# Kernel tuning notes

Measured on AMD Instinct MI355X. Metric: run time of the kernel, lower is better.

## Reference

```python
import jax, jax.numpy as jnp
import numpy as np
import math

B, L, D = 2, 2048, 1024
H, HD = 16, 64          # num heads, head dim
R = 256                 # kv lora rank = D // 4
E, K, F = 8, 2, 1024    # routed experts, top_k, intermediate size


def rmsnorm(x, w, eps=1e-6):
    ms = jnp.mean(x * x, axis=-1, keepdims=True)
    return w * (x * jax.lax.rsqrt(ms + eps))


def setup_inputs() -> dict:
    key = jax.random.key(0)
    ks = jax.random.split(key, 16)
    s = 0.02
    return {
        "x": jax.random.normal(ks[0], (B, L, D), jnp.float32),
        "ln1_w": jnp.ones((D,), jnp.float32),
        "q_w": jax.random.normal(ks[1], (D, H * HD), jnp.float32) * s,
        "kvd_w": jax.random.normal(ks[2], (D, R), jnp.float32) * s,
        "kvn_w": jnp.ones((R,), jnp.float32),
        "kvu_w": jax.random.normal(ks[3], (R, 2 * H * HD), jnp.float32) * s,
        "o_w": jax.random.normal(ks[4], (H * HD, D), jnp.float32) * s,
        "ln2_w": jnp.ones((D,), jnp.float32),
        "gate_w": jax.random.normal(ks[5], (D, E), jnp.float32) * s,
        "sh_w1": jax.random.normal(ks[6], (D, F), jnp.float32) * s,
        "sh_w2": jax.random.normal(ks[7], (F, D), jnp.float32) * s,
        "sh_w3": jax.random.normal(ks[8], (D, F), jnp.float32) * s,
        "re_w1": jax.random.normal(ks[9], (E, D, F), jnp.float32) * s,
        "re_w2": jax.random.normal(ks[10], (E, F, D), jnp.float32) * s,
        "re_w3": jax.random.normal(ks[11], (E, D, F), jnp.float32) * s,
    }


def reference(x, ln1_w, q_w, kvd_w, kvn_w, kvu_w, o_w, ln2_w, gate_w,
              sh_w1, sh_w2, sh_w3, re_w1, re_w2, re_w3):
    # ---- MLHA attention with pre-RMSNorm and latent-compressed KV ----
    xn = rmsnorm(x, ln1_w)
    q = (xn @ q_w).reshape(B, L, H, HD)
    latent = rmsnorm(xn @ kvd_w, kvn_w)                 # [B,L,R]
    kv = latent @ kvu_w                                 # [B,L,2*H*HD]
    k, v = jnp.split(kv, 2, axis=-1)
    k = k.reshape(B, L, H, HD)
    v = v.reshape(B, L, H, HD)
    scores = jnp.einsum('bxhd,byhd->bhxy', q, k) / math.sqrt(HD)
    causal = jnp.tril(jnp.ones((L, L), bool))
    scores = jnp.where(causal, scores, -jnp.inf)
    attn = jax.nn.softmax(scores, axis=-1)
    attn_out = jnp.einsum('bhxy,byhd->bxhd', attn, v).reshape(B, L, H * HD)
    h = x + attn_out @ o_w

    # ---- MoE (inference: no jitter, expert_bias = 0, no bias update) ----
    hn = rmsnorm(h, ln2_w)
    flat = hn.reshape(-1, D)                            # [T,D], T=B*L
    # shared expert (SwiGLU)
    shared = (jax.nn.silu(flat @ sh_w1) * (flat @ sh_w3)) @ sh_w2
    # router
    logits = flat @ gate_w                              # [T,E]
    probs = jax.nn.softmax(logits, axis=-1)
    topw, topi = jax.lax.top_k(probs, K)                # [T,K]
    topw = topw / jnp.sum(topw, axis=-1, keepdims=True)
    # per-token per-expert combine weight [T,E]
    combine = jnp.sum(topw[..., None] * jax.nn.one_hot(topi, E, dtype=flat.dtype), axis=1)
    # all routed experts densely, then masked combine (same math as masked loop)
    h1 = jnp.einsum('td,edf->etf', flat, re_w1)
    h3 = jnp.einsum('td,edf->etf', flat, re_w3)
    eo = jnp.einsum('etf,efd->etd', jax.nn.silu(h1) * h3, re_w2)
    routed = jnp.einsum('te,etd->td', combine, eo)
    moe_out = (shared + routed).reshape(B, L, D)
    return h + moe_out, probs
```

## Files before the change

kernel.cpp:

```cpp
#include <hip/hip_runtime.h>
#include <hip/hip_bf16.h>
#include <cstdint>
#include <cstddef>

typedef unsigned short u16;
typedef unsigned int u32;
typedef __attribute__((ext_vector_type(8))) short bf16x8;
typedef __attribute__((ext_vector_type(4))) float f32x4;

static constexpr int Bb = 2, Ll = 2048, Dd = 1024, Hh = 16, Rr = 256, Ee = 8, Ff = 1024;
static constexpr int Tt = Bb * Ll;
static constexpr float QSCALE = 0.18033688011112042f;

__device__ __forceinline__ u16 f2bf(float f){
  union { float f; u32 u; } v; v.f = f;
  u32 u = v.u;
  u32 r = u + 0x7FFFu + ((u >> 16) & 1u);
  return (u16)(r >> 16);
}
__device__ __forceinline__ float bf2f(u16 b){
  union { u32 u; float f; } v; v.u = ((u32)b) << 16; return v.f;
}

#define GLDS(gp, lp) __builtin_amdgcn_global_load_lds( \
    (const __attribute__((address_space(1))) unsigned int*)(gp), \
    (__attribute__((address_space(3))) unsigned int*)(lp), 16, 0, 0)

__global__ void transpose5(const float* __restrict__ q_w, const float* __restrict__ o_w,
                           const float* __restrict__ w1, const float* __restrict__ w3,
                           const float* __restrict__ w2,
                           u16* __restrict__ qkvdT, u16* __restrict__ oT,
                           u16* __restrict__ sh13T, u16* __restrict__ sh2T){
  const float* s; u16* d; int off, str;
  switch (blockIdx.z){
    case 0: s = q_w; d = qkvdT; off = 0; str = 1; break;
    case 1: s = o_w; d = oT;    off = 0; str = 1; break;
    case 2: s = w1;  d = sh13T; off = 0; str = 2; break;
    case 3: s = w3;  d = sh13T; off = 1; str = 2; break;
    default: s = w2; d = sh2T;  off = 0; str = 1; break;
  }
  __shared__ float tile[32][33];
  int bx = blockIdx.x * 32, by = blockIdx.y * 32;
  int tx = threadIdx.x, ty = threadIdx.y;
  #pragma unroll
  for (int i = ty; i < 32; i += 8) tile[i][tx] = s[(size_t)(by + i) * 1024 + bx + tx];
  __syncthreads();
  #pragma unroll
  for (int i = ty; i < 32; i += 8)
    d[(size_t)(off + (bx + i) * str) * 1024 + by + tx] = f2bf(tile[tx][i]);
}

__global__ void transposeEx(const float* __restrict__ re_w1, const float* __restrict__ re_w3,
                            const float* __restrict__ re_w2,
                            u16* __restrict__ re13T, u16* __restrict__ re2T){
  int z = blockIdx.z, which = z >> 3, e = z & 7;
  const float* s; u16* d; int off, str;
  size_t eo = (size_t)e * 1024 * 1024;
  if (which == 0){ s = re_w1 + eo; d = re13T + (size_t)e * 2048 * 1024; off = 0; str = 2; }
  else if (which == 1){ s = re_w3 + eo; d = re13T + (size_t)e * 2048 * 1024; off = 1; str = 2; }
  else { s = re_w2 + eo; d = re2T + (size_t)e * 1024 * 1024; off = 0; str = 1; }
  __shared__ float tile[32][33];
  int bx = blockIdx.x * 32, by = blockIdx.y * 32;
  int tx = threadIdx.x, ty = threadIdx.y;
  #pragma unroll
  for (int i = ty; i < 32; i += 8) tile[i][tx] = s[(size_t)(by + i) * 1024 + bx + tx];
  __syncthreads();
  #pragma unroll
  for (int i = ty; i < 32; i += 8)
    d[(size_t)(off + (bx + i) * str) * 1024 + by + tx] = f2bf(tile[tx][i]);
}

__global__ void transpose_conv(const float* __restrict__ src, u16* __restrict__ dst,
                               int K, int N, int dstOff){
  __shared__ float tile[32][33];
  int bx = blockIdx.x * 32, by = blockIdx.y * 32;
  int tx = threadIdx.x, ty = threadIdx.y;
  #pragma unroll
  for (int i = ty; i < 32; i += 8) tile[i][tx] = src[(size_t)(by + i) * N + bx + tx];
  __syncthreads();
  #pragma unroll
  for (int i = ty; i < 32; i += 8)
    dst[(size_t)(dstOff + bx + i) * K + by + tx] = f2bf(tile[tx][i]);
}

template<int DIM>
__global__ void rmsnorm_kernel(const float* __restrict__ x, const float* __restrict__ w,
                               u16* __restrict__ out){
  int t = blockIdx.x;
  const float* xr = x + (size_t)t * DIM;
  u16* orow = out + (size_t)t * DIM;
  int tid = threadIdx.x;
  constexpr int NT = 256;
  constexpr int PER = DIM / NT > 0 ? DIM / NT : 1;
  float vals[PER];
  float ss = 0.f;
  #pragma unroll
  for (int i = 0; i < PER; i++){
    int d = tid + i * NT;
    float v = (d < DIM) ? xr[d] : 0.f;
    vals[i] = v; ss += v * v;
  }
  __shared__ float red[4];
  for (int m = 32; m; m >>= 1) ss += __shfl_xor(ss, m, 64);
  if ((tid & 63) == 0) red[tid >> 6] = ss;
  __syncthreads();
  float tot = red[0] + red[1] + red[2] + red[3];
  float rn = rsqrtf(tot / DIM + 1e-6f);
  #pragma unroll
  for (int i = 0; i < PER; i++){
    int d = tid + i * NT;
    if (d < DIM) orow[d] = f2bf(vals[i] * rn * w[d]);
  }
}

__global__ void router_kernel(const float* __restrict__ h, const float* __restrict__ ln2w,
                              const float* __restrict__ gate,
                              float* __restrict__ probs_out,
                              int* __restrict__ topi, float* __restrict__ topw,
                              u16* __restrict__ hn){
  int t = blockIdx.x; int tid = threadIdx.x;
  const float* hr = h + (size_t)t * Dd;
  float v[4]; float ss = 0.f;
  #pragma unroll
  for (int i = 0; i < 4; i++){ float x = hr[tid + i * 256]; v[i] = x; ss += x * x; }
  __shared__ float red[4];
  for (int m = 32; m; m >>= 1) ss += __shfl_xor(ss, m, 64);
  if ((tid & 63) == 0) red[tid >> 6] = ss;
  __syncthreads();
  float rn = rsqrtf((red[0] + red[1] + red[2] + red[3]) / Dd + 1e-6f);
  float p[8];
  #pragma unroll
  for (int e = 0; e < 8; e++) p[e] = 0.f;
  #pragma unroll
  for (int i = 0; i < 4; i++){
    int d = tid + i * 256;
    float hv = v[i] * rn * ln2w[d];
    hn[(size_t)t * Dd + d] = f2bf(hv);
    const float* g = gate + (size_t)d * 8;
    #pragma unroll
    for (int e = 0; e < 8; e++) p[e] += hv * g[e];
  }
  #pragma unroll
  for (int e = 0; e < 8; e++){
    float x = p[e];
    for (int m = 32; m; m >>= 1) x += __shfl_xor(x, m, 64);
    p[e] = x;
  }
  __shared__ float pe[4][8];
  if ((tid & 63) == 0){ for (int e = 0; e < 8; e++) pe[tid >> 6][e] = p[e]; }
  __syncthreads();
  if (tid == 0){
    float lg[8];
    for (int e = 0; e < 8; e++) lg[e] = pe[0][e] + pe[1][e] + pe[2][e] + pe[3][e];
    float mx = lg[0];
    for (int e = 1; e < 8; e++) mx = fmaxf(mx, lg[e]);
    float pr[8]; float s = 0.f;
    for (int e = 0; e < 8; e++){ pr[e] = __expf(lg[e] - mx); s += pr[e]; }
    float inv = 1.f / s;
    for (int e = 0; e < 8; e++) probs_out[(size_t)t * 8 + e] = pr[e] * inv;
    int i0 = 0;
    for (int e = 1; e < 8; e++) if (pr[e] > pr[i0]) i0 = e;
    int i1 = -1;
    for (int e = 0; e < 8; e++){ if (e == i0) continue; if (i1 < 0 || pr[e] > pr[i1]) i1 = e; }
    float w0 = pr[i0], w1 = pr[i1]; float wn = 1.f / (w0 + w1);
    topi[t * 2] = i0; topi[t * 2 + 1] = i1;
    topw[t * 2] = w0 * wn; topw[t * 2 + 1] = w1 * wn;
  }
}

__global__ void hist_kernel(const int* __restrict__ topi, int* __restrict__ counts){
  __shared__ int h[8];
  int tid = threadIdx.x;
  if (tid < 8) h[tid] = 0;
  __syncthreads();
  int base = blockIdx.x * 512;
  for (int i = tid; i < 512; i += 256) atomicAdd(&h[topi[base + i]], 1);
  __syncthreads();
  if (tid < 8) atomicAdd(&counts[tid], h[tid]);
}

__global__ void bucket_kernel(const int* __restrict__ topi, const float* __restrict__ topw,
                              const int* __restrict__ counts, int* __restrict__ cur,
                              int* __restrict__ entries, float* __restrict__ ew){
  __shared__ int lh[8], lbase[8], lcur[8], loffs[8];
  int tid = threadIdx.x;
  if (tid < 8) lh[tid] = 0;
  __syncthreads();
  int t = blockIdx.x * 256 + tid;
  int e0 = topi[t * 2], e1 = topi[t * 2 + 1];
  atomicAdd(&lh[e0], 1); atomicAdd(&lh[e1], 1);
  __syncthreads();
  if (tid == 0){
    int c = 0;
    for (int e = 0; e < 8; e++){ loffs[e] = c; c += counts[e]; }
  }
  if (tid < 8){ lbase[tid] = atomicAdd(&cur[tid], lh[tid]); lcur[tid] = 0; }
  __syncthreads();
  int p0 = atomicAdd(&lcur[e0], 1);
  int pos0 = loffs[e0] + lbase[e0] + p0;
  entries[pos0] = t; ew[pos0] = topw[t * 2];
  int p1 = atomicAdd(&lcur[e1], 1);
  int pos1 = loffs[e1] + lbase[e1] + p1;
  entries[pos1] = t; ew[pos1] = topw[t * 2 + 1];
}

template<int TM, int ROWMODE, int MODE>
__launch_bounds__(256)
__global__ void gemm_bt(const u16* __restrict__ A, const u16* __restrict__ Bt,
                        void* __restrict__ C, const float* __restrict__ res,
                        int M, int N, int K, int lda, int ldc,
                        const int* __restrict__ entries, const float* __restrict__ ew,
                        const int* __restrict__ counts,
                        float* __restrict__ outAt){
  constexpr int MTC = TM / 32;
  __shared__ __align__(16) u16 As[TM * 32];
  __shared__ __align__(16) u16 Bs[128 * 32];
  __shared__ int els[TM];
  __shared__ float ewl[TM];

  int e = (ROWMODE ? blockIdx.z : 0);
  const u16* Bte = Bt + (size_t)e * N * K;
  int cnt, off;
  if (ROWMODE == 0){ cnt = M; off = 0; }
  else {
    cnt = counts[e];
    off = 0;
    for (int i = 0; i < e; i++) off += counts[i];
  }
  int rt = blockIdx.y * TM;
  if (rt >= cnt) return;
  int cb = blockIdx.x * 128;
  int tid = threadIdx.x;

  if (ROWMODE >= 1){
    if (tid < TM){
      int r = rt + tid;
      els[tid] = (r < cnt) ? entries[off + r] : 0;
      ewl[tid] = (MODE == 4 && r < cnt) ? ew[off + r] : 0.f;
    }
    __syncthreads();
  }

  int sr = tid >> 2;
  int skc = (tid & 3) * 8;
  int rr0 = rt + sr, rr1 = rt + sr + 64;
  size_t ar0 = 0, ar1 = 0;
  if (ROWMODE == 0){ ar0 = (size_t)rr0; ar1 = (size_t)rr1; }
  else if (ROWMODE == 1){ ar0 = (size_t)els[sr];
                          ar1 = (TM == 128) ? (size_t)els[sr + 64] : 0; }
  else {
    int c0 = rr0 < cnt ? rr0 : (cnt - 1);
    int c1 = rr1 < cnt ? rr1 : (cnt - 1);
    ar0 = (size_t)off + c0; ar1 = (size_t)off + c1;
  }
  const u16* pa0 = A + ar0 * lda + skc;
  const u16* pa1 = A + ar1 * lda + skc;
  const u16* pb0 = Bte + (size_t)(cb + sr) * K + skc;
  const u16* pb1 = Bte + (size_t)(cb + sr + 64) * K + skc;
  u16* lA0 = &As[tid * 8];
  u16* lA1 = &As[(TM == 128 ? 2048 : 0) + tid * 8];
  u16* lB0 = &Bs[tid * 8];
  u16* lB1 = &Bs[2048 + tid * 8];

  int w = tid >> 6, lane = tid & 63;
  int wm = w >> 1, wn = w & 1;
  int quad = lane >> 4, l16 = lane & 15;

  f32x4 acc[MTC][4];
  const f32x4 zf = {0.f, 0.f, 0.f, 0.f};
  #pragma unroll
  for (int i = 0; i < MTC; i++)
    #pragma unroll
    for (int j = 0; j < 4; j++) acc[i][j] = zf;

  for (int k0 = 0; k0 < K; k0 += 32){
    __syncthreads();
    GLDS(pa0 + k0, lA0);
    if (TM == 128) GLDS(pa1 + k0, lA1);
    GLDS(pb0 + k0, lB0);
    GLDS(pb1 + k0, lB1);
    __syncthreads();
    bf16x8 af[MTC], bfr[4];
    #pragma unroll
    for (int mt = 0; mt < MTC; mt++)
      af[mt] = *(const bf16x8*)&As[(wm * (TM / 2) + mt * 16 + l16) * 32 + quad * 8];
    #pragma unroll
    for (int nt = 0; nt < 4; nt++)
      bfr[nt] = *(const bf16x8*)&Bs[(wn * 64 + nt * 16 + l16) * 32 + quad * 8];
    #pragma unroll
    for (int mt = 0; mt < MTC; mt++)
      #pragma unroll
      for (int nt = 0; nt < 4; nt++)
        acc[mt][nt] = __builtin_amdgcn_mfma_f32_16x16x32_bf16(af[mt], bfr[nt], acc[mt][nt], 0, 0, 0);
  }

  #pragma unroll
  for (int mt = 0; mt < MTC; mt++){
    #pragma unroll
    for (int nt = 0; nt < 4; nt++){
      #pragma unroll
      for (int r = 0; r < 4; r++){
        int row = wm * (TM / 2) + mt * 16 + quad * 4 + r;
        int col = cb + wn * 64 + nt * 16 + l16;
        int rr = rt + row;
        float v = acc[mt][nt][r];
        if (MODE == 6){
          float pv = __shfl_xor(v, 1, 64);
          if (rr < cnt && (l16 & 1) == 0){
            float sl = v / (1.f + __expf(-v));
            size_t crow = (size_t)((ROWMODE == 1) ? (off + rr) : rr);
            ((u16*)C)[crow * ldc + (col >> 1)] = f2bf(sl * pv);
          }
          continue;
        }
        if (rr >= cnt) continue;
        if (MODE == 0){
          size_t ci = (size_t)((ROWMODE == 1) ? (off + rr) : rr) * ldc + col;
          ((u16*)C)[ci] = f2bf(v);
        } else if (MODE == 1){
          size_t ci = (size_t)rr * ldc + col;
          ((float*)C)[ci] = v + res[ci];
        } else if (MODE == 5){
          if (col < 1024) ((u16*)C)[(size_t)rr * 1024 + col] = f2bf(v * QSCALE);
          else            outAt[(size_t)rr * 256 + (col - 1024)] = v;
        } else {
          int tok = els[row];
          atomicAdd(&outAt[(size_t)tok * ldc + col], ewl[row] * v);
        }
      }
    }
  }
}

__global__ void vt_kernel(const u16* __restrict__ kv, u16* __restrict__ vt){
  __shared__ __align__(16) u16 t[64 * 72];
  int kt = blockIdx.x * 64, h = blockIdx.y, b = blockIdx.z;
  size_t bL = (size_t)b * Ll;
  int tid = threadIdx.x;
  int r = tid >> 2, c0 = (tid & 3) * 16;
  const u16* src = kv + (bL + kt + r) * 2048 + 1024 + h * 64 + c0;
  *(uint4*)&t[r * 72 + c0]     = *(const uint4*)(src);
  *(uint4*)&t[r * 72 + c0 + 8] = *(const uint4*)(src + 8);
  __syncthreads();
  int d = tid >> 2; int k0 = (tid & 3) * 16;
  u16 tmp[16];
  #pragma unroll
  for (int j = 0; j < 16; j++) tmp[j] = t[(k0 + j) * 72 + d];
  u16* dst = vt + ((size_t)(b * Hh + h) * 64 + d) * (size_t)Ll + kt + k0;
  *(uint4*)dst       = *(const uint4*)&tmp[0];
  *(uint4*)(dst + 8) = *(const uint4*)&tmp[8];
}

__launch_bounds__(256)
__global__ void attn_kernel(const u16* __restrict__ q, const u16* __restrict__ kv,
                            const u16* __restrict__ vt, u16* __restrict__ out){
  constexpr int LD = 72;
  __shared__ __align__(16) u16 Ks[2][64 * LD];
  __shared__ __align__(16) u16 Vs[2][64 * LD];
  __shared__ __align__(16) u16 Ps[64 * LD];
  int h = blockIdx.y, b = blockIdx.z;
  size_t bL = (size_t)b * Ll;
  int tid = threadIdx.x, w = tid >> 6, lane = tid & 63, quad = lane >> 4, l16 = lane & 15;
  int sr = tid >> 2, sc = (tid & 3) * 16;
  const u16* kbase = kv + (bL + sr) * 2048 + h * 64 + sc;
  const u16* vbase = vt + ((size_t)(b * Hh + h) * 64 + sr) * (size_t)Ll + sc;
  const f32x4 zf = {0.f, 0.f, 0.f, 0.f};

  #pragma unroll
  for (int pass = 0; pass < 2; pass++){
    int q0 = (pass ? (31 - (int)blockIdx.x) : (int)blockIdx.x) * 64;
    int qrow = q0 + w * 16 + l16;

    bf16x8 qf[2];
    #pragma unroll
    for (int ks = 0; ks < 2; ks++)
      qf[ks] = *(const bf16x8*)(q + (bL + qrow) * 1024 + h * 64 + ks * 32 + quad * 8);

    f32x4 oacc[4];
    #pragma unroll
    for (int dt = 0; dt < 4; dt++) oacc[dt] = zf;
    float mprev = -1e30f, lsum = 0.f;

    uint4 kr0 = *(const uint4*)(kbase);
    uint4 kr1 = *(const uint4*)(kbase + 8);
    uint4 vr0 = *(const uint4*)(vbase);
    uint4 vr1 = *(const uint4*)(vbase + 8);
    *(uint4*)&Ks[0][sr * LD + sc]     = kr0;
    *(uint4*)&Ks[0][sr * LD + sc + 8] = kr1;
    *(uint4*)&Vs[0][sr * LD + sc]     = vr0;
    *(uint4*)&Vs[0][sr * LD + sc + 8] = vr1;
    int cur = 0;
    __syncthreads();

    for (int kt = 0; kt <= q0; kt += 64){
      bool pfetch = (kt + 64 <= q0);
      if (pfetch){
        const u16* kp = kbase + (size_t)(kt + 64) * 2048;
        kr0 = *(const uint4*)(kp);
        kr1 = *(const uint4*)(kp + 8);
        const u16* vp = vbase + kt + 64;
        vr0 = *(const uint4*)(vp);
        vr1 = *(const uint4*)(vp + 8);
      }
      const u16* ksp = Ks[cur];
      const u16* vsp = Vs[cur];

      f32x4 sacc[4];
      #pragma unroll
      for (int mt = 0; mt < 4; mt++) sacc[mt] = zf;
      __builtin_amdgcn_s_setprio(1);
      #pragma unroll
      for (int ks = 0; ks < 2; ks++){
        #pragma unroll
        for (int mt = 0; mt < 4; mt++){
          bf16x8 kf = *(const bf16x8*)&ksp[(mt * 16 + l16) * LD + ks * 32 + quad * 8];
          sacc[mt] = __builtin_amdgcn_mfma_f32_16x16x32_bf16(kf, qf[ks], sacc[mt], 0, 0, 0);
        }
      }
      __builtin_amdgcn_s_setprio(0);

      bool diag = (kt == q0);
      int lq = w * 16 + l16;
      float sv[16]; float mx = -1e30f;
      #pragma unroll
      for (int mt = 0; mt < 4; mt++){
        #pragma unroll
        for (int r = 0; r < 4; r++){
          float s = sacc[mt][r];
          if (diag && (mt * 16 + quad * 4 + r > lq)) s = -1e30f;
          sv[mt * 4 + r] = s;
          mx = fmaxf(mx, s);
        }
      }
      mx = fmaxf(mx, __shfl_xor(mx, 16, 64));
      mx = fmaxf(mx, __shfl_xor(mx, 32, 64));
      if (!__all(mx <= mprev)){
        float mnew = fmaxf(mprev, mx);
        float alpha = exp2f(mprev - mnew);
        mprev = mnew;
        lsum *= alpha;
        #pragma unroll
        for (int dt = 0; dt < 4; dt++) oacc[dt] *= alpha;
      }
      float rs = 0.f;
      #pragma unroll
      for (int mt = 0; mt < 4; mt++){
        float p0 = exp2f(sv[mt * 4 + 0] - mprev);
        float p1 = exp2f(sv[mt * 4 + 1] - mprev);
        float p2 = exp2f(sv[mt * 4 + 2] - mprev);
        float p3 = exp2f(sv[mt * 4 + 3] - mprev);
        rs += p0 + p1 + p2 + p3;
        union { uint2 u; __hip_bfloat162 h2[2]; } pk;
        pk.h2[0] = __float22bfloat162_rn(make_float2(p0, p1));
        pk.h2[1] = __float22bfloat162_rn(make_float2(p2, p3));
        *(uint2*)&Ps[(w * 16 + l16) * LD + mt * 16 + quad * 4] = pk.u;
      }
      rs += __shfl_xor(rs, 16, 64);
      rs += __shfl_xor(rs, 32, 64);
      lsum += rs;

      __builtin_amdgcn_s_setprio(1);
      #pragma unroll
      for (int ks = 0; ks < 2; ks++){
        bf16x8 pfr = *(const bf16x8*)&Ps[(w * 16 + l16) * LD + ks * 32 + quad * 8];
        #pragma unroll
        for (int dt = 0; dt < 4; dt++){
          bf16x8 vf = *(const bf16x8*)&vsp[(dt * 16 + l16) * LD + ks * 32 + quad * 8];
          oacc[dt] = __builtin_amdgcn_mfma_f32_16x16x32_bf16(vf, pfr, oacc[dt], 0, 0, 0);
        }
      }
      __builtin_amdgcn_s_setprio(0);

      if (pfetch){
        int nb = cur ^ 1;
        *(uint4*)&Ks[nb][sr * LD + sc]     = kr0;
        *(uint4*)&Ks[nb][sr * LD + sc + 8] = kr1;
        *(uint4*)&Vs[nb][sr * LD + sc]     = vr0;
        *(uint4*)&Vs[nb][sr * LD + sc + 8] = vr1;
        cur = nb;
      }
      __syncthreads();
    }

    float inv = 1.f / lsum;
    #pragma unroll
    for (int dt = 0; dt < 4; dt++){
      union { uint2 u; __hip_bfloat162 h2[2]; } ov;
      ov.h2[0] = __float22bfloat162_rn(make_float2(oacc[dt][0] * inv, oacc[dt][1] * inv));
      ov.h2[1] = __float22bfloat162_rn(make_float2(oacc[dt][2] * inv, oacc[dt][3] * inv));
      *(uint2*)(out + (bL + qrow) * 1024 + h * 64 + dt * 16 + quad * 4) = ov.u;
    }
  }
}

extern "C" void kernel_launch(void* const* d_in, const int* in_sizes, int n_in,
                              void* d_out, int out_size, void* d_ws, size_t ws_size,
                              hipStream_t stream){
  const float* x     = (const float*)d_in[0];
  const float* ln1_w = (const float*)d_in[1];
  const float* q_w   = (const float*)d_in[2];
  const float* kvd_w = (const float*)d_in[3];
  const float* kvn_w = (const float*)d_in[4];
  const float* kvu_w = (const float*)d_in[5];
  const float* o_w   = (const float*)d_in[6];
  const float* ln2_w = (const float*)d_in[7];
  const float* gate_w= (const float*)d_in[8];
  const float* sh_w1 = (const float*)d_in[9];
  const float* sh_w2 = (const float*)d_in[10];
  const float* sh_w3 = (const float*)d_in[11];
  const float* re_w1 = (const float*)d_in[12];
  const float* re_w2 = (const float*)d_in[13];
  const float* re_w3 = (const float*)d_in[14];
  float* out = (float*)d_out;

  char* wp = (char*)d_ws;
  auto alloc = [&](size_t bytes)->char*{
    char* p = wp; wp += (bytes + 255) & ~(size_t)255; return p;
  };
  u16* qkvdT = (u16*)alloc((size_t)1280 * 1024 * 2);
  u16* kvuT  = (u16*)alloc((size_t)2048 * 256 * 2);
  u16* oT    = (u16*)alloc((size_t)1024 * 1024 * 2);
  u16* sh13T = (u16*)alloc((size_t)2048 * 1024 * 2);
  u16* sh2T  = (u16*)alloc((size_t)1024 * 1024 * 2);
  u16* re13T = (u16*)alloc((size_t)8 * 2048 * 1024 * 2);
  u16* re2T  = (u16*)alloc((size_t)8 * 1024 * 1024 * 2);
  u16* xn    = (u16*)alloc((size_t)Tt * 1024 * 2);
  u16* qbuf  = (u16*)alloc((size_t)Tt * 1024 * 2);
  float* latpre = (float*)alloc((size_t)Tt * 256 * 4);
  u16* lat   = (u16*)alloc((size_t)Tt * 256 * 2);
  u16* kvbuf = (u16*)alloc((size_t)Tt * 2048 * 2);
  u16* attnb = (u16*)alloc((size_t)Tt * 1024 * 2);
  float* hbuf = (float*)alloc((size_t)Tt * 1024 * 4);
  u16* vtb   = (u16*)alloc((size_t)Bb * Hh * 64 * Ll * 2);
  u16* gr    = (u16*)alloc((size_t)Tt * 2 * 1024 * 2);
  int* counts = (int*)alloc(32);
  int* cur    = (int*)alloc(32);
  int* topi   = (int*)alloc((size_t)Tt * 2 * 4);
  float* topw = (float*)alloc((size_t)Tt * 2 * 4);
  int* entries= (int*)alloc((size_t)Tt * 2 * 4);
  float* ewt  = (float*)alloc((size_t)Tt * 2 * 4);
  (void)ws_size; (void)n_in; (void)in_sizes; (void)out_size;

  hipMemsetAsync(counts, 0, 32, stream);
  hipMemsetAsync(cur, 0, 32, stream);

  dim3 tb(32, 8);
  transpose5<<<dim3(32, 32, 5), tb, 0, stream>>>(q_w, o_w, sh_w1, sh_w3, sh_w2,
                                                 qkvdT, oT, sh13T, sh2T);
  transpose_conv<<<dim3(8, 32, 1), tb, 0, stream>>>(kvd_w, qkvdT, 1024, 256, 1024);
  transpose_conv<<<dim3(64, 8, 1), tb, 0, stream>>>(kvu_w, kvuT, 256, 2048, 0);
  transposeEx<<<dim3(32, 32, 24), tb, 0, stream>>>(re_w1, re_w3, re_w2, re13T, re2T);

  rmsnorm_kernel<1024><<<Tt, 256, 0, stream>>>(x, ln1_w, xn);

  gemm_bt<64,0,5><<<dim3(10, 64), 256, 0, stream>>>(xn, qkvdT, qbuf, nullptr,
      Tt, 1280, 1024, 1024, 1024, nullptr, nullptr, nullptr, latpre);
  rmsnorm_kernel<256><<<Tt, 256, 0, stream>>>(latpre, kvn_w, lat);
  gemm_bt<128,0,0><<<dim3(16, 32), 256, 0, stream>>>(lat, kvuT, kvbuf, nullptr,
      Tt, 2048, 256, 256, 2048, nullptr, nullptr, nullptr, nullptr);
  vt_kernel<<<dim3(32, 16, 2), 256, 0, stream>>>(kvbuf, vtb);
  attn_kernel<<<dim3(16, 16, 2), 256, 0, stream>>>(qbuf, kvbuf, vtb, attnb);
  gemm_bt<64,0,1><<<dim3(8, 64), 256, 0, stream>>>(attnb, oT, hbuf, x,
      Tt, 1024, 1024, 1024, 1024, nullptr, nullptr, nullptr, nullptr);
  router_kernel<<<Tt, 256, 0, stream>>>(hbuf, ln2_w, gate_w, out + (size_t)Tt * Dd,
                                        topi, topw, xn);
  hist_kernel<<<16, 256, 0, stream>>>(topi, counts);
  bucket_kernel<<<16, 256, 0, stream>>>(topi, topw, counts, cur, entries, ewt);

  gemm_bt<128,0,6><<<dim3(16, 32), 256, 0, stream>>>(xn, sh13T, kvbuf, nullptr,
      Tt, 2048, 1024, 1024, 1024, nullptr, nullptr, nullptr, nullptr);
  gemm_bt<64,0,1><<<dim3(8, 64), 256, 0, stream>>>(kvbuf, sh2T, out, hbuf,
      Tt, 1024, 1024, 1024, 1024, nullptr, nullptr, nullptr, nullptr);

  gemm_bt<128,1,6><<<dim3(16, 32, 8), 256, 0, stream>>>(xn, re13T, gr, nullptr,
      Tt, 2048, 1024, 1024, 1024, entries, nullptr, counts, nullptr);
  gemm_bt<128,2,4><<<dim3(8, 32, 8), 256, 0, stream>>>(gr, re2T, nullptr, nullptr,
      Tt, 1024, 1024, 1024, 1024, entries, ewt, counts, out);
}
```

Baseline: 560.2 us.

## Merge shared and routed SwiGLU up-projections into one 256x256-tile MFMA kernel

```diff
diff --git a/kernel.cpp b/kernel.cpp
--- a/kernel.cpp
+++ b/kernel.cpp
@@ -332,6 +332,163 @@
   }
 }
 
+#define RBAR() __builtin_amdgcn_s_barrier()
+#define MMQ(MQ, NQ, FA, FB) do{ \
+  _Pragma("unroll") \
+  for (int m4_ = 0; m4_ < 4; m4_++){ \
+    _Pragma("unroll") \
+    for (int n2_ = 0; n2_ < 2; n2_++){ \
+      acc[(MQ)*4+m4_][(NQ)*2+n2_] = __builtin_amdgcn_mfma_f32_16x16x32_bf16(FA[m4_][0], FB[n2_][0], acc[(MQ)*4+m4_][(NQ)*2+n2_], 0, 0, 0); \
+      acc[(MQ)*4+m4_][(NQ)*2+n2_] = __builtin_amdgcn_mfma_f32_16x16x32_bf16(FA[m4_][1], FB[n2_][1], acc[(MQ)*4+m4_][(NQ)*2+n2_], 0, 0, 0); \
+    } \
+  } }while(0)
+#define RDA(DST, BB, MQ) do{ \
+  _Pragma("unroll") \
+  for (int m4_ = 0; m4_ < 4; m4_++){ \
+    const char* p_ = (const char*)(&As[BB][0]) + (size_t)(wm*128 + (MQ)*64 + m4_*16 + l16)*128; \
+    DST[m4_][0] = *(const bf16x8*)(p_ + offk0); \
+    DST[m4_][1] = *(const bf16x8*)(p_ + offk1); \
+  } }while(0)
+#define RDB(DST, BB, NQ) do{ \
+  _Pragma("unroll") \
+  for (int n2_ = 0; n2_ < 2; n2_++){ \
+    const char* p_ = (const char*)(&Bs[BB][0]) + (size_t)(wn*64 + (NQ)*32 + n2_*16 + l16)*128; \
+    DST[n2_][0] = *(const bf16x8*)(p_ + offk0); \
+    DST[n2_][1] = *(const bf16x8*)(p_ + offk1); \
+  } }while(0)
+#define STGA(SB, H, KT) do{ \
+  GLDS(gA[(H)*2+0] + (size_t)(KT)*64, &As[SB][((H)*128 +  0)*64] + (size_t)tid*8); \
+  GLDS(gA[(H)*2+1] + (size_t)(KT)*64, &As[SB][((H)*128 + 64)*64] + (size_t)tid*8); }while(0)
+#define STGB(SB, H, KT) do{ \
+  GLDS(gB[(H)*2+0] + (size_t)(KT)*64, &Bs[SB][((H)*128 +  0)*64] + (size_t)tid*8); \
+  GLDS(gB[(H)*2+1] + (size_t)(KT)*64, &Bs[SB][((H)*128 + 64)*64] + (size_t)tid*8); }while(0)
+
+__launch_bounds__(512, 2)
+__global__ void gemm256_up(const u16* __restrict__ A,
+                           const u16* __restrict__ sh13, const u16* __restrict__ re13,
+                           u16* __restrict__ shg, u16* __restrict__ gr,
+                           const int* __restrict__ entries, const int* __restrict__ counts){
+  __shared__ __align__(16) u16 As[2][256 * 64];
+  __shared__ __align__(16) u16 Bs[2][256 * 64];
+
+  int e = blockIdx.z;
+  int cnt, off = 0;
+  if (e < 8){
+    cnt = counts[e];
+    for (int i = 0; i < e; i++) off += counts[i];
+  } else cnt = Tt;
+  int rt = blockIdx.y * 256;
+  if (rt >= cnt) return;
+  int cb = blockIdx.x * 256;
+  const u16* Bte = (e < 8) ? (re13 + (size_t)e * 2048 * 1024) : sh13;
+  u16* Cb = (e < 8) ? gr : shg;
+
+  int tid = threadIdx.x;
+  int w = tid >> 6, lane = tid & 63, quad = lane >> 4, l16 = lane & 15;
+  int wm = w >> 2, wn = w & 3;
+  int swz = (l16 & 7) << 4;
+  int offk0 = (quad * 16) ^ swz;
+  int offk1 = (64 + quad * 16) ^ swz;
+
+  int trow = tid >> 3;
+  int sk = ((((tid & 7) << 4) ^ ((trow & 7) << 4)) >> 1);
+  const u16* gA[4]; const u16* gB[4];
+  #pragma unroll
+  for (int i = 0; i < 4; i++){
+    int r = i * 64 + trow;
+    int garow;
+    if (e < 8){
+      int idx = rt + r; if (idx >= cnt) idx = cnt - 1;
+      garow = entries[off + idx];
+    } else garow = rt + r;
+    gA[i] = A + (size_t)garow * 1024 + sk;
+    gB[i] = Bte + (size_t)(cb + r) * 1024 + sk;
+  }
+
+  f32x4 acc[8][4];
+  const f32x4 zf = {0.f, 0.f, 0.f, 0.f};
+  #pragma unroll
+  for (int i = 0; i < 8; i++)
+    #pragma unroll
+    for (int j = 0; j < 4; j++) acc[i][j] = zf;
+
+  STGB(0, 0, 0); STGB(0, 1, 0);
+  STGA(0, 0, 0); STGA(0, 1, 0);
+  __syncthreads();
+
+  bf16x8 fa0[4][2], fa1[4][2], fb0[2][2], fb1[2][2];
+
+  for (int it = 0; it < 8; ++it){
+    int t1 = 2 * it + 1, t2 = 2 * it + 2;
+    RDA(fa0, 0, 0); RDB(fb0, 0, 0);
+    STGB(1, 0, t1);
+    RBAR();
+    __builtin_amdgcn_s_setprio(1); MMQ(0, 0, fa0, fb0); __builtin_amdgcn_s_setprio(0);
+    RBAR();
+
+    RDB(fb1, 0, 1);
+    STGB(1, 1, t1);
+    RBAR();
+    __builtin_amdgcn_s_setprio(1); MMQ(0, 1, fa0, fb1); __builtin_amdgcn_s_setprio(0);
+    RBAR();
+
+    RDA(fa1, 0, 1);
+    STGA(1, 0, t1);
+    RBAR();
+    __builtin_amdgcn_s_setprio(1); MMQ(1, 0, fa1, fb0); __builtin_amdgcn_s_setprio(0);
+    RBAR();
+
+    STGA(1, 1, t1);
+    RBAR();
+    __builtin_amdgcn_s_setprio(1); MMQ(1, 1, fa1, fb1); __builtin_amdgcn_s_setprio(0);
+    __syncthreads();
+
+    bool pf = (it < 7);
+    RDA(fa0, 1, 0); RDB(fb0, 1, 0);
+    if (pf) STGB(0, 0, t2);
+    RBAR();
+    __builtin_amdgcn_s_setprio(1); MMQ(0, 0, fa0, fb0); __builtin_amdgcn_s_setprio(0);
+    RBAR();
+
+    RDB(fb1, 1, 1);
+    if (pf) STGB(0, 1, t2);
+    RBAR();
+    __builtin_amdgcn_s_setprio(1); MMQ(0, 1, fa0, fb1); __builtin_amdgcn_s_setprio(0);
+    RBAR();
+
+    RDA(fa1, 1, 1);
+    if (pf) STGA(0, 0, t2);
+    RBAR();
+    __builtin_amdgcn_s_setprio(1); MMQ(1, 0, fa1, fb0); __builtin_amdgcn_s_setprio(0);
+    RBAR();
+
+    if (pf) STGA(0, 1, t2);
+    RBAR();
+    __builtin_amdgcn_s_setprio(1); MMQ(1, 1, fa1, fb1); __builtin_amdgcn_s_setprio(0);
+    __syncthreads();
+  }
+
+  #pragma unroll
+  for (int mi = 0; mi < 8; mi++){
+    #pragma unroll
+    for (int ni = 0; ni < 4; ni++){
+      #pragma unroll
+      for (int r = 0; r < 4; r++){
+        int row = wm * 128 + (mi >> 2) * 64 + (mi & 3) * 16 + quad * 4 + r;
+        int col = cb + wn * 64 + (ni >> 1) * 32 + (ni & 1) * 16 + l16;
+        float v = acc[mi][ni][r];
+        float pv = __shfl_xor(v, 1, 64);
+        int grow = rt + row;
+        if (grow < cnt && (l16 & 1) == 0){
+          float sl = v / (1.f + __expf(-v));
+          size_t crow = (e < 8) ? (size_t)(off + grow) : (size_t)grow;
+          Cb[crow * 1024 + (col >> 1)] = f2bf(sl * pv);
+        }
+      }
+    }
+  }
+}
+
 __global__ void vt_kernel(const u16* __restrict__ kv, u16* __restrict__ vt){
   __shared__ __align__(16) u16 t[64 * 72];
   int kt = blockIdx.x * 64, h = blockIdx.y, b = blockIdx.z;
@@ -567,13 +724,11 @@
   hist_kernel<<<16, 256, 0, stream>>>(topi, counts);
   bucket_kernel<<<16, 256, 0, stream>>>(topi, topw, counts, cur, entries, ewt);
 
-  gemm_bt<128,0,6><<<dim3(16, 32), 256, 0, stream>>>(xn, sh13T, kvbuf, nullptr,
-      Tt, 2048, 1024, 1024, 1024, nullptr, nullptr, nullptr, nullptr);
+  gemm256_up<<<dim3(8, 16, 9), 512, 0, stream>>>(xn, sh13T, re13T, kvbuf, gr,
+                                                 entries, counts);
+
   gemm_bt<64,0,1><<<dim3(8, 64), 256, 0, stream>>>(kvbuf, sh2T, out, hbuf,
       Tt, 1024, 1024, 1024, 1024, nullptr, nullptr, nullptr, nullptr);
-
-  gemm_bt<128,1,6><<<dim3(16, 32, 8), 256, 0, stream>>>(xn, re13T, gr, nullptr,
-      Tt, 2048, 1024, 1024, 1024, entries, nullptr, counts, nullptr);
   gemm_bt<128,2,4><<<dim3(8, 32, 8), 256, 0, stream>>>(gr, re2T, nullptr, nullptr,
       Tt, 1024, 1024, 1024, 1024, entries, ewt, counts, out);
 }
```

New measurement: 548.9 us. -2.0%, faster.
